# Performance work log

Measured on AMD Instinct MI355X. Metric: run time of the kernel, lower is better.

## Reference

```python
import jax, jax.numpy as jnp
import numpy as np

N = 50000
E = 800000
EC = 200000
L = 128
PD = 3
IN_MAIN = 2 * L + 2 * (PD + 1)   # 264
IN_CONT = 2 * L + PD + 1          # 260
IN_NODE = 3 * L                   # 384
EPS = 1e-5


def _ln(h):
    # LayerNorm over last dim, no affine params
    m = jnp.mean(h, axis=-1, keepdims=True)
    v = jnp.mean(jnp.square(h - m), axis=-1, keepdims=True)
    return (h - m) * jax.lax.rsqrt(v + EPS)


def _mlp(h, W0, b0, W1, b1, W2, b2):
    # 2 hidden ReLU layers + output Linear + LayerNorm(no affine)
    h = jax.nn.relu(h @ W0 + b0)
    h = jax.nn.relu(h @ W1 + b1)
    return _ln(h @ W2 + b2)


def _mp(x, idx, pos, pos_w, use_mat, W0, b0, W1, b1, W2, b2):
    i, j = idx[0], idx[1]
    x_i = x[i]
    x_j = x[j]
    feats = []
    if use_mat:
        d = pos[i] - pos[j]
        feats += [d, jnp.linalg.norm(d, axis=-1, keepdims=True)]
    dw = pos_w[i] - pos_w[j]
    feats += [dw, jnp.linalg.norm(dw, axis=-1, keepdims=True)]
    tmp = jnp.concatenate(feats + [x_i, x_j], axis=-1)
    emb = _mlp(tmp, W0, b0, W1, b1, W2, b2)
    return jax.ops.segment_sum(emb, j, num_segments=N)


def _lin(key, fan_in, fan_out):
    k1, k2 = jax.random.split(key)
    bd = 1.0 / np.sqrt(fan_in)
    W = jax.random.uniform(k1, (fan_in, fan_out), jnp.float32, -bd, bd)
    b = jax.random.uniform(k2, (fan_out,), jnp.float32, -bd, bd)
    return W, b


def setup_inputs() -> dict:
    key = jax.random.key(0)
    ks = jax.random.split(key, 16)
    inp = {
        "x": jax.random.normal(ks[0], (N, L), jnp.float32),
        "g": jax.random.randint(ks[1], (2, E), 0, N, jnp.int32),
        "cg": jax.random.randint(ks[2], (2, EC), 0, N, jnp.int32),
        "pos_posw": jax.random.normal(ks[3], (N, 2 * PD), jnp.float32),
    }
    dims = {"main": IN_MAIN, "cont": IN_CONT, "node": IN_NODE}
    kidx = 4
    for name, in_dim in dims.items():
        fi = in_dim
        for l in range(3):
            W, b = _lin(ks[kidx], fi, L)
            inp[f"{name}_W{l}"] = W
            inp[f"{name}_b{l}"] = b
            fi = L
            kidx += 1
    return inp


def reference(x, g, cg, pos_posw,
              main_W0, main_b0, main_W1, main_b1, main_W2, main_b2,
              cont_W0, cont_b0, cont_W1, cont_b1, cont_W2, cont_b2,
              node_W0, node_b0, node_W1, node_b1, node_W2, node_b2):
    D = pos_posw.shape[-1] // 2
    pos, pos_w = pos_posw[:, :D], pos_posw[:, D:]
    agg_main = _mp(x, g, pos, pos_w, True,
                   main_W0, main_b0, main_W1, main_b1, main_W2, main_b2)
    agg_cont = _mp(x, cg, pos, pos_w, False,
                   cont_W0, cont_b0, cont_W1, cont_b1, cont_W2, cont_b2)
    tmp = jnp.concatenate([x, agg_main, agg_cont], axis=-1)
    return _mlp(tmp, node_W0, node_b0, node_W1, node_b1, node_W2, node_b2) + x
```

## Files before the change

### kernel.cpp

```cpp
#include <hip/hip_runtime.h>
#include <hip/hip_bf16.h>

#define NN 50000
#define NE_MAIN 800000
#define NE_CONT 200000
#define NP 50176

typedef __attribute__((ext_vector_type(8))) short bf8;
typedef __attribute__((ext_vector_type(4))) float f4;

static __device__ __forceinline__ float bf2f(short s) {
  return __builtin_bit_cast(float, ((unsigned int)(unsigned short)s) << 16);
}
static __device__ __forceinline__ short f2bf(float f) {
  __hip_bfloat16 h = __float2bfloat16(f);
  return __builtin_bit_cast(short, h);
}

static __device__ __forceinline__ int xcd_swizzle(int bid, int nwg) {
  int xcd = bid & 7;
  int q = nwg >> 3, r = nwg & 7;
  int base = (xcd < r) ? xcd * (q + 1) : r * (q + 1) + (xcd - r) * q;
  return base + (bid >> 3);
}

__global__ __launch_bounds__(256) void zero2_kernel(f4* __restrict__ p0, int n0,
                                                    f4* __restrict__ p1, int n1) {
  int i = blockIdx.x * 256 + threadIdx.x;
  int stride = gridDim.x * 256;
  f4 z = {0.f, 0.f, 0.f, 0.f};
  for (int k = i; k < n0; k += stride) p0[k] = z;
  for (int k = i; k < n1; k += stride) p1[k] = z;
}

__global__ __launch_bounds__(256) void hist2_kernel(const int* __restrict__ gm,
                                                    const int* __restrict__ gc,
                                                    int* __restrict__ hm,
                                                    int* __restrict__ hc, int bm) {
  if ((int)blockIdx.x < bm) {
    int e = blockIdx.x * 256 + threadIdx.x;
    int st = bm * 256;
    for (; e < NE_MAIN; e += st) atomicAdd(&hm[gm[NE_MAIN + e]], 1);
  } else {
    int e = (blockIdx.x - bm) * 256 + threadIdx.x;
    int st = (gridDim.x - bm) * 256;
    for (; e < NE_CONT; e += st) atomicAdd(&hc[gc[NE_CONT + e]], 1);
  }
}

__global__ __launch_bounds__(512) void scan1_kernel(const int* __restrict__ hm,
                                                    int* __restrict__ cm, int* __restrict__ tm,
                                                    const int* __restrict__ hc,
                                                    int* __restrict__ cc, int* __restrict__ tc,
                                                    int n, int nt) {
  __shared__ int buf[2][512];
  const int set = (int)blockIdx.x >= nt;
  const int* hist = set ? hc : hm;
  int* cursor = set ? cc : cm;
  int* tsums  = set ? tc : tm;
  const int blk = set ? blockIdx.x - nt : blockIdx.x;
  int tid = threadIdx.x;
  int i = blk * 512 + tid;
  int v = (i < n) ? hist[i] : 0;
  int cur = 0;
  buf[0][tid] = v;
  __syncthreads();
#pragma unroll
  for (int off = 1; off < 512; off <<= 1) {
    int t = buf[cur][tid];
    if (tid >= off) t += buf[cur][tid - off];
    buf[cur ^ 1][tid] = t;
    cur ^= 1;
    __syncthreads();
  }
  int incl = buf[cur][tid];
  if (i < n) cursor[i] = incl - v;
  if (tid == 511) tsums[blk] = incl;
}

__global__ __launch_bounds__(512) void scan2_kernel(int* __restrict__ tm,
                                                    int* __restrict__ tc, int nt) {
  __shared__ int buf[2][512];
  int* tsums = blockIdx.x ? tc : tm;
  int tid = threadIdx.x;
  int v = (tid < nt) ? tsums[tid] : 0;
  int cur = 0;
  buf[0][tid] = v;
  __syncthreads();
#pragma unroll
  for (int off = 1; off < 512; off <<= 1) {
    int t = buf[cur][tid];
    if (tid >= off) t += buf[cur][tid - off];
    buf[cur ^ 1][tid] = t;
    cur ^= 1;
    __syncthreads();
  }
  if (tid < nt) tsums[tid] = buf[cur][tid] - v;
}

__global__ __launch_bounds__(512) void scan3_kernel(int* __restrict__ cm,
                                                    const int* __restrict__ tm,
                                                    int* __restrict__ cc,
                                                    const int* __restrict__ tc,
                                                    int n, int nt) {
  const int set = (int)blockIdx.x >= nt;
  int* cursor = set ? cc : cm;
  const int* tsums = set ? tc : tm;
  const int blk = set ? blockIdx.x - nt : blockIdx.x;
  int i = blk * 512 + threadIdx.x;
  if (i < n) cursor[i] += tsums[blk];
}

__global__ __launch_bounds__(256) void scatter2_kernel(const int* __restrict__ gm,
                                                       const int* __restrict__ gc,
                                                       int* __restrict__ cm, int* __restrict__ cc,
                                                       int* __restrict__ sim, int* __restrict__ sjm,
                                                       int* __restrict__ sic, int* __restrict__ sjc,
                                                       int bm) {
  if ((int)blockIdx.x < bm) {
    int e = blockIdx.x * 256 + threadIdx.x;
    int st = bm * 256;
    for (; e < NE_MAIN; e += st) {
      int i = gm[e], j = gm[NE_MAIN + e];
      int p = atomicAdd(&cm[j], 1);
      sim[p] = i; sjm[p] = j;
    }
  } else {
    int e = (blockIdx.x - bm) * 256 + threadIdx.x;
    int st = (gridDim.x - bm) * 256;
    for (; e < NE_CONT; e += st) {
      int i = gc[e], j = gc[NE_CONT + e];
      int p = atomicAdd(&cc[j], 1);
      sic[p] = i; sjc[p] = j;
    }
  }
}

struct WTDesc {
  const float* src[11];
  int K[11];
  int off[11];
};
__global__ __launch_bounds__(128) void wt_kernel(WTDesc d, short* __restrict__ dst) {
  int m = blockIdx.x >> 7;
  int n = blockIdx.x & 127;
  const float* s = d.src[m];
  int K = d.K[m];
  short* o = dst + d.off[m] + (size_t)n * K;
  for (int k = threadIdx.x; k < K; k += 128) o[k] = f2bf(s[(size_t)k * 128 + n]);
}

template <int K>
static __device__ __forceinline__ void mfma_gemm(const short* __restrict__ sA, int rs16,
                                                 const short* __restrict__ WT,
                                                 int c0, int lane,
                                                 const float* __restrict__ bias,
                                                 f4 (&acc)[4][2]) {
  const int colA = c0 + (lane & 15);
  const int colB = colA + 16;
  if (bias) {
    float ba = bias[colA], bb = bias[colB];
#pragma unroll
    for (int rf = 0; rf < 4; ++rf) {
      acc[rf][0] = (f4){ba, ba, ba, ba};
      acc[rf][1] = (f4){bb, bb, bb, bb};
    }
  } else {
#pragma unroll
    for (int rf = 0; rf < 4; ++rf) {
      acc[rf][0] = (f4){0.f, 0.f, 0.f, 0.f};
      acc[rf][1] = (f4){0.f, 0.f, 0.f, 0.f};
    }
  }
  const int g = lane >> 4;
  const int rowl = lane & 15;
#pragma unroll 4
  for (int ks = 0; ks < (K >> 5); ++ks) {
    bf8 b0 = *reinterpret_cast<const bf8*>(WT + (size_t)colA * K + ks * 32 + g * 8);
    bf8 b1 = *reinterpret_cast<const bf8*>(WT + (size_t)colB * K + ks * 32 + g * 8);
    int chunk = ks * 4 + g;
#pragma unroll
    for (int rf = 0; rf < 4; ++rf) {
      int row = rf * 16 + rowl;
      bf8 a = *reinterpret_cast<const bf8*>(sA + row * rs16 * 8 + ((chunk ^ (row & 7)) << 3));
      acc[rf][0] = __builtin_amdgcn_mfma_f32_16x16x32_bf16(a, b0, acc[rf][0], 0, 0, 0);
      acc[rf][1] = __builtin_amdgcn_mfma_f32_16x16x32_bf16(a, b1, acc[rf][1], 0, 0, 0);
    }
  }
}

template <bool RELU, bool SWZ>
static __device__ __forceinline__ void store_frags(short* __restrict__ dst, int rs16,
                                                   int c0, int lane, const f4 (&acc)[4][2]) {
#pragma unroll
  for (int rf = 0; rf < 4; ++rf)
#pragma unroll
    for (int q = 0; q < 4; ++q) {
      int row = rf * 16 + ((lane >> 4) << 2) + q;
#pragma unroll
      for (int cf = 0; cf < 2; ++cf) {
        int col = c0 + cf * 16 + (lane & 15);
        float v = acc[rf][cf][q];
        if (RELU) v = fmaxf(v, 0.f);
        int idx;
        if (SWZ) idx = row * rs16 * 8 + (((col >> 3) ^ (row & 7)) << 3) + (col & 7);
        else     idx = row * rs16 * 8 + col;
        dst[idx] = f2bf(v);
      }
    }
}

static __device__ __forceinline__ void ln_rows(const f4 (&acc)[4][2], int lane, int wave,
                                               float2* __restrict__ sP) {
#pragma unroll
  for (int rf = 0; rf < 4; ++rf)
#pragma unroll
    for (int q = 0; q < 4; ++q) {
      float v0 = acc[rf][0][q], v1 = acc[rf][1][q];
      float s = v0 + v1;
      float qq = v0 * v0 + v1 * v1;
      s += __shfl_xor(s, 1);  qq += __shfl_xor(qq, 1);
      s += __shfl_xor(s, 2);  qq += __shfl_xor(qq, 2);
      s += __shfl_xor(s, 4);  qq += __shfl_xor(qq, 4);
      s += __shfl_xor(s, 8);  qq += __shfl_xor(qq, 8);
      if ((lane & 15) == 0) {
        int row = rf * 16 + ((lane >> 4) << 2) + q;
        sP[wave * 64 + row] = make_float2(s, qq);
      }
    }
}

__global__ __launch_bounds__(256) void precompute_kernel(
    const float* __restrict__ x, const short* __restrict__ WTp,
    const float* __restrict__ mb0, const float* __restrict__ cb0,
    short* __restrict__ xa_m, short* __restrict__ xb_m,
    short* __restrict__ xa_c, short* __restrict__ xb_c) {
  __shared__ __align__(16) short sA[64 * 128];
  __shared__ __align__(16) short sOut[64 * 128];
  const int tid = threadIdx.x;
  const int lane = tid & 63, wave = tid >> 6;
  const int c0 = wave * 32;
  const int n0 = blockIdx.x * 64;

#pragma unroll
  for (int it = 0; it < 4; ++it) {
    int s = it * 256 + tid;
    int e = s >> 4, c = s & 15;
    int n = n0 + e;
    f4 u0 = {0.f, 0.f, 0.f, 0.f}, u1 = {0.f, 0.f, 0.f, 0.f};
    if (n < NN) {
      u0 = *reinterpret_cast<const f4*>(x + (size_t)n * 128 + c * 8);
      u1 = *reinterpret_cast<const f4*>(x + (size_t)n * 128 + c * 8 + 4);
    }
    bf8 o;
#pragma unroll
    for (int j = 0; j < 4; ++j) { o[j] = f2bf(u0[j]); o[j + 4] = f2bf(u1[j]); }
    *reinterpret_cast<bf8*>(sA + e * 128 + ((c ^ (e & 7)) << 3)) = o;
  }
  __syncthreads();

  short* dsts[4] = {xa_m, xb_m, xa_c, xb_c};
  const float* biases[4] = {nullptr, mb0, nullptr, cb0};
#pragma unroll 1
  for (int o = 0; o < 4; ++o) {
    f4 acc[4][2];
    mfma_gemm<128>(sA, 16, WTp + o * 16384, c0, lane, biases[o], acc);
    store_frags<false, false>(sOut, 16, c0, lane, acc);
    __syncthreads();
    short* dst = dsts[o];
#pragma unroll
    for (int it = 0; it < 4; ++it) {
      int s = it * 256 + tid;
      int e = s >> 4, c = s & 15;
      int n = n0 + e;
      if (n < NN)
        *reinterpret_cast<bf8*>(dst + (size_t)n * 128 + c * 8) =
            *reinterpret_cast<const bf8*>(sOut + e * 128 + c * 8);
    }
    __syncthreads();
  }
}

template <int NF>
__global__ __launch_bounds__(256) void edge_kernel(
    const int* __restrict__ si, const int* __restrict__ sjv,
    const float* __restrict__ pp,
    const short* __restrict__ xa, const short* __restrict__ xb,
    const float* __restrict__ W0f,
    const short* __restrict__ WT1, const float* __restrict__ b1v,
    const short* __restrict__ WT2, const float* __restrict__ b2v,
    float* __restrict__ agg) {
  __shared__ __align__(16) short sA[64 * 128];
  __shared__ int sI[64], sJ[64];
  __shared__ float sF[64][NF];
  __shared__ float2 sP[4 * 64];
  __shared__ float2 sStats[64];
  const int tid = threadIdx.x;
  const int lane = tid & 63, wave = tid >> 6;
  const int c0 = wave * 32;
  const int base = xcd_swizzle(blockIdx.x, gridDim.x) * 64;

  if (tid < 64) {
    int e = base + tid;
    int i = si[e], j = sjv[e];
    sI[tid] = i; sJ[tid] = j;
    const float* pi = pp + (size_t)i * 6;
    const float* pj = pp + (size_t)j * 6;
    if (NF == 8) {
      float d0 = pi[0] - pj[0], d1 = pi[1] - pj[1], d2 = pi[2] - pj[2];
      sF[tid][0] = d0; sF[tid][1] = d1; sF[tid][2] = d2;
      sF[tid][3] = sqrtf(d0 * d0 + d1 * d1 + d2 * d2);
      float w0 = pi[3] - pj[3], w1 = pi[4] - pj[4], w2 = pi[5] - pj[5];
      sF[tid][4] = w0; sF[tid][5] = w1; sF[tid][6] = w2;
      sF[tid][7] = sqrtf(w0 * w0 + w1 * w1 + w2 * w2);
    } else {
      float w0 = pi[3] - pj[3], w1 = pi[4] - pj[4], w2 = pi[5] - pj[5];
      sF[tid][0] = w0; sF[tid][1] = w1; sF[tid][2] = w2;
      sF[tid][3] = sqrtf(w0 * w0 + w1 * w1 + w2 * w2);
    }
  }
  __syncthreads();

#pragma unroll
  for (int it = 0; it < 4; ++it) {
    int s = it * 256 + tid;
    int e = s >> 4, c = s & 15;
    bf8 va = *reinterpret_cast<const bf8*>(xa + (size_t)sI[e] * 128 + c * 8);
    bf8 vb = *reinterpret_cast<const bf8*>(xb + (size_t)sJ[e] * 128 + c * 8);
    float h[8];
#pragma unroll
    for (int jj = 0; jj < 8; ++jj) h[jj] = bf2f(va[jj]) + bf2f(vb[jj]);
#pragma unroll
    for (int q = 0; q < NF; ++q) {
      float fq = sF[e][q];
      f4 w0 = *reinterpret_cast<const f4*>(W0f + q * 128 + c * 8);
      f4 w1 = *reinterpret_cast<const f4*>(W0f + q * 128 + c * 8 + 4);
#pragma unroll
      for (int jj = 0; jj < 4; ++jj) {
        h[jj]     = fmaf(fq, w0[jj], h[jj]);
        h[jj + 4] = fmaf(fq, w1[jj], h[jj + 4]);
      }
    }
    bf8 o;
#pragma unroll
    for (int jj = 0; jj < 8; ++jj) o[jj] = f2bf(fmaxf(h[jj], 0.f));
    *reinterpret_cast<bf8*>(sA + e * 128 + ((c ^ (e & 7)) << 3)) = o;
  }
  __syncthreads();

  f4 acc[4][2];
  mfma_gemm<128>(sA, 16, WT1, c0, lane, b1v, acc);
  __syncthreads();
  store_frags<true, true>(sA, 16, c0, lane, acc);
  __syncthreads();
  mfma_gemm<128>(sA, 16, WT2, c0, lane, b2v, acc);
  ln_rows(acc, lane, wave, sP);
  __syncthreads();
  if (tid < 64) {
    float s = 0.f, qq = 0.f;
#pragma unroll
    for (int w = 0; w < 4; ++w) { s += sP[w * 64 + tid].x; qq += sP[w * 64 + tid].y; }
    float mean = s * (1.f / 128.f);
    float var = qq * (1.f / 128.f) - mean * mean;
    sStats[tid] = make_float2(mean, rsqrtf(var + 1e-5f));
  }
  __syncthreads();

#pragma unroll
  for (int rf = 0; rf < 4; ++rf)
#pragma unroll
    for (int q = 0; q < 4; ++q) {
      int row = rf * 16 + ((lane >> 4) << 2) + q;
      float mean = sStats[row].x, rn = sStats[row].y;
#pragma unroll
      for (int cf = 0; cf < 2; ++cf) {
        int col = c0 + cf * 16 + (lane & 15);
        sA[row * 128 + ((col + 4 * row) & 127)] = f2bf((acc[rf][cf][q] - mean) * rn);
      }
    }
  __syncthreads();

  {
    int grp = tid >> 7, c = tid & 127;
    int r0g = grp * 32;
    float accum = 0.f;
#pragma unroll 4
    for (int rr = r0g; rr < r0g + 32; ++rr) {
      accum += bf2f(sA[rr * 128 + ((c + 4 * rr) & 127)]);
      bool flush = (rr == r0g + 31) || (sJ[rr + 1] != sJ[rr]);
      if (flush) {
        unsafeAtomicAdd(agg + (size_t)sJ[rr] * 128 + c, accum);
        accum = 0.f;
      }
    }
  }
}

__global__ __launch_bounds__(256) void node_kernel(
    const float* __restrict__ x,
    const float* __restrict__ agg_m, const float* __restrict__ agg_c,
    const short* __restrict__ WT0, const float* __restrict__ b0v,
    const short* __restrict__ WT1, const float* __restrict__ b1v,
    const short* __restrict__ WT2, const float* __restrict__ b2v,
    float* __restrict__ out) {
  __shared__ __align__(16) short sA[64 * 384];
  __shared__ float2 sP[4 * 64];
  __shared__ float2 sStats[64];
  const int tid = threadIdx.x;
  const int lane = tid & 63, wave = tid >> 6;
  const int c0 = wave * 32;
  const int n0 = blockIdx.x * 64;

#pragma unroll
  for (int p = 0; p < 3; ++p) {
    const float* src = (p == 0) ? x : (p == 1) ? agg_m : agg_c;
#pragma unroll
    for (int it = 0; it < 4; ++it) {
      int s = it * 256 + tid;
      int e = s >> 4, cl = s & 15;
      int n = n0 + e;
      f4 u0 = {0.f, 0.f, 0.f, 0.f}, u1 = {0.f, 0.f, 0.f, 0.f};
      if (n < NN) {
        u0 = *reinterpret_cast<const f4*>(src + (size_t)n * 128 + cl * 8);
        u1 = *reinterpret_cast<const f4*>(src + (size_t)n * 128 + cl * 8 + 4);
      }
      bf8 o;
#pragma unroll
      for (int j = 0; j < 4; ++j) { o[j] = f2bf(u0[j]); o[j + 4] = f2bf(u1[j]); }
      int c = p * 16 + cl;
      *reinterpret_cast<bf8*>(sA + e * 384 + ((c ^ (e & 7)) << 3)) = o;
    }
  }
  __syncthreads();

  f4 acc[4][2];
  mfma_gemm<384>(sA, 48, WT0, c0, lane, b0v, acc);
  __syncthreads();
  store_frags<true, true>(sA, 16, c0, lane, acc);
  __syncthreads();
  mfma_gemm<128>(sA, 16, WT1, c0, lane, b1v, acc);
  __syncthreads();
  store_frags<true, true>(sA + 8192, 16, c0, lane, acc);
  __syncthreads();
  mfma_gemm<128>(sA + 8192, 16, WT2, c0, lane, b2v, acc);

  ln_rows(acc, lane, wave, sP);
  __syncthreads();
  if (tid < 64) {
    float s = 0.f, qq = 0.f;
#pragma unroll
    for (int w = 0; w < 4; ++w) { s += sP[w * 64 + tid].x; qq += sP[w * 64 + tid].y; }
    float mean = s * (1.f / 128.f);
    float var = qq * (1.f / 128.f) - mean * mean;
    sStats[tid] = make_float2(mean, rsqrtf(var + 1e-5f));
  }
  __syncthreads();

#pragma unroll
  for (int rf = 0; rf < 4; ++rf)
#pragma unroll
    for (int q = 0; q < 4; ++q) {
      int row = rf * 16 + ((lane >> 4) << 2) + q;
      int n = n0 + row;
      if (n < NN) {
        float mean = sStats[row].x, rn = sStats[row].y;
#pragma unroll
        for (int cf = 0; cf < 2; ++cf) {
          int col = c0 + cf * 16 + (lane & 15);
          float xv = x[(size_t)n * 128 + col];
          out[(size_t)n * 128 + col] = (acc[rf][cf][q] - mean) * rn + xv;
        }
      }
    }
}

extern "C" void kernel_launch(void* const* d_in, const int* in_sizes, int n_in,
                              void* d_out, int out_size, void* d_ws, size_t ws_size,
                              hipStream_t stream) {
  const float* x   = (const float*)d_in[0];
  const int*   g   = (const int*)d_in[1];
  const int*   cgr = (const int*)d_in[2];
  const float* pp  = (const float*)d_in[3];
  const float* mW0 = (const float*)d_in[4];
  const float* mb0 = (const float*)d_in[5];
  const float* mW1 = (const float*)d_in[6];
  const float* mb1 = (const float*)d_in[7];
  const float* mW2 = (const float*)d_in[8];
  const float* mb2 = (const float*)d_in[9];
  const float* cW0 = (const float*)d_in[10];
  const float* cb0 = (const float*)d_in[11];
  const float* cW1 = (const float*)d_in[12];
  const float* cb1 = (const float*)d_in[13];
  const float* cW2 = (const float*)d_in[14];
  const float* cb2 = (const float*)d_in[15];
  const float* nW0 = (const float*)d_in[16];
  const float* nb0 = (const float*)d_in[17];
  const float* nW1 = (const float*)d_in[18];
  const float* nb1 = (const float*)d_in[19];
  const float* nW2 = (const float*)d_in[20];
  const float* nb2 = (const float*)d_in[21];
  float* out = (float*)d_out;

  WTDesc d;
  const float* srcs[11] = {mW1, mW2, cW1, cW2, nW0, nW1, nW2,
                           mW0 + 8 * 128, mW0 + 136 * 128, cW0 + 4 * 128, cW0 + 132 * 128};
  int Ks[11] = {128, 128, 128, 128, 384, 128, 128, 128, 128, 128, 128};
  int off = 0;
  for (int m = 0; m < 11; ++m) { d.src[m] = srcs[m]; d.K[m] = Ks[m]; d.off[m] = off; off += Ks[m] * 128; }

  char* ws = (char*)d_ws;
  const size_t TBL = (size_t)NN * 128 * 2;
  const size_t AGG = (size_t)NN * 128 * 4;
  short* xa_m = (short*)(ws);
  short* xb_m = (short*)(ws + TBL);
  short* xa_c = (short*)(ws + 2 * TBL);
  short* xb_c = (short*)(ws + 3 * TBL);
  float* agg_m = (float*)(ws + 4 * TBL);
  float* agg_c = (float*)(ws + 4 * TBL + AGG);
  short* wt = (short*)(ws + 4 * TBL + 2 * AGG);
  char* ib = ws + 4 * TBL + 2 * AGG + (size_t)off * 2;
  int* hist_m   = (int*)(ib);
  int* hist_c   = hist_m + NP;
  int* cursor_m = hist_c + NP;
  int* cursor_c = cursor_m + NP;
  int* tsum_m   = cursor_c + NP;
  int* tsum_c   = tsum_m + 128;
  int* si_m     = tsum_c + 128;
  int* sj_m     = si_m + NE_MAIN;
  int* si_c     = sj_m + NE_MAIN;
  int* sj_c     = si_c + NE_CONT;

  short* wt1_m = wt + d.off[0];
  short* wt2_m = wt + d.off[1];
  short* wt1_c = wt + d.off[2];
  short* wt2_c = wt + d.off[3];
  short* wtn0  = wt + d.off[4];
  short* wtn1  = wt + d.off[5];
  short* wtn2  = wt + d.off[6];
  short* wtp   = wt + d.off[7];

  const int NT = (NN + 511) / 512;

  wt_kernel<<<11 * 128, 128, 0, stream>>>(d, wt);
  zero2_kernel<<<2048, 256, 0, stream>>>((f4*)agg_m, (int)(2 * (size_t)NN * 128 / 4),
                                         (f4*)hist_m, 2 * NP / 4);

  hist2_kernel<<<1024 + 256, 256, 0, stream>>>(g, cgr, hist_m, hist_c, 1024);
  scan1_kernel<<<2 * NT, 512, 0, stream>>>(hist_m, cursor_m, tsum_m,
                                           hist_c, cursor_c, tsum_c, NN, NT);
  scan2_kernel<<<2, 512, 0, stream>>>(tsum_m, tsum_c, NT);
  scan3_kernel<<<2 * NT, 512, 0, stream>>>(cursor_m, tsum_m, cursor_c, tsum_c, NN, NT);
  scatter2_kernel<<<1024 + 256, 256, 0, stream>>>(g, cgr, cursor_m, cursor_c,
                                                  si_m, sj_m, si_c, sj_c, 1024);

  precompute_kernel<<<(NN + 63) / 64, 256, 0, stream>>>(x, wtp, mb0, cb0,
                                                        xa_m, xb_m, xa_c, xb_c);

  edge_kernel<8><<<NE_MAIN / 64, 256, 0, stream>>>(si_m, sj_m, pp, xa_m, xb_m,
                                                   mW0, wt1_m, mb1, wt2_m, mb2, agg_m);
  edge_kernel<4><<<NE_CONT / 64, 256, 0, stream>>>(si_c, sj_c, pp, xa_c, xb_c,
                                                   cW0, wt1_c, cb1, wt2_c, cb2, agg_c);

  node_kernel<<<(NN + 63) / 64, 256, 0, stream>>>(x, agg_m, agg_c,
                                                  wtn0, nb0, wtn1, nb1, wtn2, nb2, out);
}
```

Baseline: 657.5 us.

## Restructure edge kernel so each wave owns 16 edges without block barriers

The edge MLP kernel is rewritten so each wave independently handles 16 edges. It gathers node features straight into MFMA A-fragments in registers and reads B-fragments of the weights directly from global memory rather than through a shared 64-row tile. LayerNorm statistics are reduced with cross-lane shuffles instead of shared-memory partial sums, and all block-wide __syncthreads are removed in favour of per-wave shared scratch. The small first-layer positional weights are pre-converted to bf16 by a new tiny kernel. The trade-off is that every wave now reloads the full weight matrices from global memory or cache, and the segment-sum runs over 16-edge groups, which can produce more atomics.

```diff
diff --git a/kernel.cpp b/kernel.cpp
--- a/kernel.cpp
+++ b/kernel.cpp
@@ -150,6 +150,15 @@
   for (int k = threadIdx.x; k < K; k += 128) o[k] = f2bf(s[(size_t)k * 128 + n]);
 }
 
+__global__ __launch_bounds__(256) void cvtw0f_kernel(const float* __restrict__ mW0,
+                                                     const float* __restrict__ cW0,
+                                                     short* __restrict__ w0f_m,
+                                                     short* __restrict__ w0f_c) {
+  int t = blockIdx.x * 256 + threadIdx.x;
+  if (t < 8 * 128) w0f_m[t] = f2bf(mW0[t]);
+  if (t < 4 * 128) w0f_c[t] = f2bf(cW0[t]);
+}
+
 template <int K>
 static __device__ __forceinline__ void mfma_gemm(const short* __restrict__ sA, int rs16,
                                                  const short* __restrict__ WT,
@@ -286,110 +295,139 @@
     const int* __restrict__ si, const int* __restrict__ sjv,
     const float* __restrict__ pp,
     const short* __restrict__ xa, const short* __restrict__ xb,
-    const float* __restrict__ W0f,
+    const short* __restrict__ W0fb,
     const short* __restrict__ WT1, const float* __restrict__ b1v,
     const short* __restrict__ WT2, const float* __restrict__ b2v,
     float* __restrict__ agg) {
-  __shared__ __align__(16) short sA[64 * 128];
-  __shared__ int sI[64], sJ[64];
-  __shared__ float sF[64][NF];
-  __shared__ float2 sP[4 * 64];
-  __shared__ float2 sStats[64];
+  __shared__ __align__(16) short sH[4][16 * 128];
+  __shared__ int sJw[4][20];
   const int tid = threadIdx.x;
   const int lane = tid & 63, wave = tid >> 6;
-  const int c0 = wave * 32;
-  const int base = xcd_swizzle(blockIdx.x, gridDim.x) * 64;
-
-  if (tid < 64) {
-    int e = base + tid;
-    int i = si[e], j = sjv[e];
-    sI[tid] = i; sJ[tid] = j;
-    const float* pi = pp + (size_t)i * 6;
-    const float* pj = pp + (size_t)j * 6;
+  const int g = lane >> 4, r = lane & 15;
+  short* Hs = sH[wave];
+  int* Jw = sJw[wave];
+
+  const int base = (xcd_swizzle(blockIdx.x, gridDim.x) * 4 + wave) * 16;
+  const int e = base + r;
+  const int i = si[e];
+  const int j = sjv[e];
+  if (lane < 16) Jw[lane] = j;
+
+  const float* pi = pp + (size_t)i * 6;
+  const float* pj = pp + (size_t)j * 6;
+  float feat[NF];
+  {
+    float w0 = pi[3] - pj[3], w1 = pi[4] - pj[4], w2 = pi[5] - pj[5];
     if (NF == 8) {
       float d0 = pi[0] - pj[0], d1 = pi[1] - pj[1], d2 = pi[2] - pj[2];
-      sF[tid][0] = d0; sF[tid][1] = d1; sF[tid][2] = d2;
-      sF[tid][3] = sqrtf(d0 * d0 + d1 * d1 + d2 * d2);
-      float w0 = pi[3] - pj[3], w1 = pi[4] - pj[4], w2 = pi[5] - pj[5];
-      sF[tid][4] = w0; sF[tid][5] = w1; sF[tid][6] = w2;
-      sF[tid][7] = sqrtf(w0 * w0 + w1 * w1 + w2 * w2);
+      feat[0] = d0; feat[1] = d1; feat[2] = d2;
+      feat[3] = sqrtf(d0 * d0 + d1 * d1 + d2 * d2);
+      feat[4] = w0; feat[5] = w1; feat[6] = w2;
+      feat[7] = sqrtf(w0 * w0 + w1 * w1 + w2 * w2);
     } else {
-      float w0 = pi[3] - pj[3], w1 = pi[4] - pj[4], w2 = pi[5] - pj[5];
-      sF[tid][0] = w0; sF[tid][1] = w1; sF[tid][2] = w2;
-      sF[tid][3] = sqrtf(w0 * w0 + w1 * w1 + w2 * w2);
-    }
-  }
-  __syncthreads();
-
-#pragma unroll
-  for (int it = 0; it < 4; ++it) {
-    int s = it * 256 + tid;
-    int e = s >> 4, c = s & 15;
-    bf8 va = *reinterpret_cast<const bf8*>(xa + (size_t)sI[e] * 128 + c * 8);
-    bf8 vb = *reinterpret_cast<const bf8*>(xb + (size_t)sJ[e] * 128 + c * 8);
+      feat[0] = w0; feat[1] = w1; feat[2] = w2;
+      feat[3] = sqrtf(w0 * w0 + w1 * w1 + w2 * w2);
+    }
+  }
+
+  bf8 afr[4];
+#pragma unroll
+  for (int ks = 0; ks < 4; ++ks) {
+    int ko = ks * 32 + g * 8;
+    bf8 va = *reinterpret_cast<const bf8*>(xa + (size_t)i * 128 + ko);
+    bf8 vb = *reinterpret_cast<const bf8*>(xb + (size_t)j * 128 + ko);
     float h[8];
 #pragma unroll
     for (int jj = 0; jj < 8; ++jj) h[jj] = bf2f(va[jj]) + bf2f(vb[jj]);
 #pragma unroll
     for (int q = 0; q < NF; ++q) {
-      float fq = sF[e][q];
-      f4 w0 = *reinterpret_cast<const f4*>(W0f + q * 128 + c * 8);
-      f4 w1 = *reinterpret_cast<const f4*>(W0f + q * 128 + c * 8 + 4);
-#pragma unroll
-      for (int jj = 0; jj < 4; ++jj) {
-        h[jj]     = fmaf(fq, w0[jj], h[jj]);
-        h[jj + 4] = fmaf(fq, w1[jj], h[jj + 4]);
-      }
+      bf8 w = *reinterpret_cast<const bf8*>(W0fb + q * 128 + ko);
+#pragma unroll
+      for (int jj = 0; jj < 8; ++jj) h[jj] = fmaf(feat[q], bf2f(w[jj]), h[jj]);
     }
     bf8 o;
 #pragma unroll
     for (int jj = 0; jj < 8; ++jj) o[jj] = f2bf(fmaxf(h[jj], 0.f));
-    *reinterpret_cast<bf8*>(sA + e * 128 + ((c ^ (e & 7)) << 3)) = o;
-  }
-  __syncthreads();
-
-  f4 acc[4][2];
-  mfma_gemm<128>(sA, 16, WT1, c0, lane, b1v, acc);
-  __syncthreads();
-  store_frags<true, true>(sA, 16, c0, lane, acc);
-  __syncthreads();
-  mfma_gemm<128>(sA, 16, WT2, c0, lane, b2v, acc);
-  ln_rows(acc, lane, wave, sP);
-  __syncthreads();
-  if (tid < 64) {
-    float s = 0.f, qq = 0.f;
-#pragma unroll
-    for (int w = 0; w < 4; ++w) { s += sP[w * 64 + tid].x; qq += sP[w * 64 + tid].y; }
-    float mean = s * (1.f / 128.f);
-    float var = qq * (1.f / 128.f) - mean * mean;
-    sStats[tid] = make_float2(mean, rsqrtf(var + 1e-5f));
-  }
-  __syncthreads();
-
-#pragma unroll
-  for (int rf = 0; rf < 4; ++rf)
+    afr[ks] = o;
+  }
+
+  f4 acc[8];
+#pragma unroll
+  for (int cf = 0; cf < 8; ++cf) {
+    int col = cf * 16 + r;
+    float bb = b1v[col];
+    acc[cf] = (f4){bb, bb, bb, bb};
+#pragma unroll
+    for (int ks = 0; ks < 4; ++ks) {
+      bf8 b = *reinterpret_cast<const bf8*>(WT1 + (size_t)col * 128 + ks * 32 + g * 8);
+      acc[cf] = __builtin_amdgcn_mfma_f32_16x16x32_bf16(afr[ks], b, acc[cf], 0, 0, 0);
+    }
+  }
+
+#pragma unroll
+  for (int cf = 0; cf < 8; ++cf)
 #pragma unroll
     for (int q = 0; q < 4; ++q) {
-      int row = rf * 16 + ((lane >> 4) << 2) + q;
-      float mean = sStats[row].x, rn = sStats[row].y;
-#pragma unroll
-      for (int cf = 0; cf < 2; ++cf) {
-        int col = c0 + cf * 16 + (lane & 15);
-        sA[row * 128 + ((col + 4 * row) & 127)] = f2bf((acc[rf][cf][q] - mean) * rn);
-      }
-    }
-  __syncthreads();
-
-  {
-    int grp = tid >> 7, c = tid & 127;
-    int r0g = grp * 32;
+      int row = g * 4 + q;
+      int col = cf * 16 + r;
+      int chunk = ((col >> 3) + row) & 15;
+      Hs[row * 128 + chunk * 8 + (col & 7)] = f2bf(fmaxf(acc[cf][q], 0.f));
+    }
+  bf8 afr2[4];
+#pragma unroll
+  for (int ks = 0; ks < 4; ++ks) {
+    int chunk = (ks * 4 + g + r) & 15;
+    afr2[ks] = *reinterpret_cast<const bf8*>(Hs + r * 128 + chunk * 8);
+  }
+
+#pragma unroll
+  for (int cf = 0; cf < 8; ++cf) {
+    int col = cf * 16 + r;
+    float bb = b2v[col];
+    acc[cf] = (f4){bb, bb, bb, bb};
+#pragma unroll
+    for (int ks = 0; ks < 4; ++ks) {
+      bf8 b = *reinterpret_cast<const bf8*>(WT2 + (size_t)col * 128 + ks * 32 + g * 8);
+      acc[cf] = __builtin_amdgcn_mfma_f32_16x16x32_bf16(afr2[ks], b, acc[cf], 0, 0, 0);
+    }
+  }
+
+  float mean[4], rn[4];
+#pragma unroll
+  for (int q = 0; q < 4; ++q) {
+    float s = 0.f, ss = 0.f;
+#pragma unroll
+    for (int cf = 0; cf < 8; ++cf) { float v = acc[cf][q]; s += v; ss += v * v; }
+    s += __shfl_xor(s, 1);  ss += __shfl_xor(ss, 1);
+    s += __shfl_xor(s, 2);  ss += __shfl_xor(ss, 2);
+    s += __shfl_xor(s, 4);  ss += __shfl_xor(ss, 4);
+    s += __shfl_xor(s, 8);  ss += __shfl_xor(ss, 8);
+    mean[q] = s * (1.f / 128.f);
+    float var = ss * (1.f / 128.f) - mean[q] * mean[q];
+    rn[q] = rsqrtf(var + 1e-5f);
+  }
+
+#pragma unroll
+  for (int cf = 0; cf < 8; ++cf)
+#pragma unroll
+    for (int q = 0; q < 4; ++q) {
+      int row = g * 4 + q;
+      int col = cf * 16 + r;
+      int chunk = ((col >> 3) + row) & 15;
+      Hs[row * 128 + chunk * 8 + (col & 7)] = f2bf((acc[cf][q] - mean[q]) * rn[q]);
+    }
+
+#pragma unroll
+  for (int half = 0; half < 2; ++half) {
+    int c = lane + half * 64;
     float accum = 0.f;
 #pragma unroll 4
-    for (int rr = r0g; rr < r0g + 32; ++rr) {
-      accum += bf2f(sA[rr * 128 + ((c + 4 * rr) & 127)]);
-      bool flush = (rr == r0g + 31) || (sJ[rr + 1] != sJ[rr]);
+    for (int rr = 0; rr < 16; ++rr) {
+      int chunk = ((c >> 3) + rr) & 15;
+      accum += bf2f(Hs[rr * 128 + chunk * 8 + (c & 7)]);
+      bool flush = (rr == 15) || (Jw[rr + 1] != Jw[rr]);
       if (flush) {
-        unsafeAtomicAdd(agg + (size_t)sJ[rr] * 128 + c, accum);
+        unsafeAtomicAdd(agg + (size_t)Jw[rr] * 128 + c, accum);
         accum = 0.f;
       }
     }
@@ -518,7 +556,9 @@
   float* agg_m = (float*)(ws + 4 * TBL);
   float* agg_c = (float*)(ws + 4 * TBL + AGG);
   short* wt = (short*)(ws + 4 * TBL + 2 * AGG);
-  char* ib = ws + 4 * TBL + 2 * AGG + (size_t)off * 2;
+  short* w0f_m = wt + off;
+  short* w0f_c = w0f_m + 8 * 128;
+  char* ib = (char*)(w0f_c + 4 * 128 + 64);
   int* hist_m   = (int*)(ib);
   int* hist_c   = hist_m + NP;
   int* cursor_m = hist_c + NP;
@@ -542,6 +582,7 @@
   const int NT = (NN + 511) / 512;
 
   wt_kernel<<<11 * 128, 128, 0, stream>>>(d, wt);
+  cvtw0f_kernel<<<4, 256, 0, stream>>>(mW0, cW0, w0f_m, w0f_c);
   zero2_kernel<<<2048, 256, 0, stream>>>((f4*)agg_m, (int)(2 * (size_t)NN * 128 / 4),
                                          (f4*)hist_m, 2 * NP / 4);
 
@@ -557,9 +598,9 @@
                                                         xa_m, xb_m, xa_c, xb_c);
 
   edge_kernel<8><<<NE_MAIN / 64, 256, 0, stream>>>(si_m, sj_m, pp, xa_m, xb_m,
-                                                   mW0, wt1_m, mb1, wt2_m, mb2, agg_m);
+                                                   w0f_m, wt1_m, mb1, wt2_m, mb2, agg_m);
   edge_kernel<4><<<NE_CONT / 64, 256, 0, stream>>>(si_c, sj_c, pp, xa_c, xb_c,
-                                                   cW0, wt1_c, cb1, wt2_c, cb2, agg_c);
+                                                   w0f_c, wt1_c, cb1, wt2_c, cb2, agg_c);
 
   node_kernel<<<(NN + 63) / 64, 256, 0, stream>>>(x, agg_m, agg_c,
                                                   wtn0, nb0, wtn1, nb1, wtn2, nb2, out);
```

After: 881.1 us. 1.34x slower.
